# Performance work log

Hardware: AMD Instinct MI355X
Metric: run time of the kernel (lower is better)

## Reference

```python
import jax, jax.numpy as jnp
import numpy as np


def setup_inputs() -> dict:
    key = jax.random.key(0)
    kq, kk, kv, kl = jax.random.split(key, 4)
    B, H, S, D = 2, 8, 1024, 64
    Q = jax.random.normal(kq, (B, H, S, D), dtype=jnp.float32)
    K = jax.random.normal(kk, (B, H, S, D), dtype=jnp.float32)
    V = jax.random.normal(kv, (B, H, S, D), dtype=jnp.float32)
    valid_lens = jax.random.randint(kl, (B, S), 0, S, dtype=jnp.int64)
    return {"Q": Q, "K": K, "V": V, "valid_lens": valid_lens}


def reference(Q, K, V, valid_lens):
    # Q,K,V: [B,H,S,D]. The torch repeat/reshape makes K[b,i,j]=K[b,j],
    # i.e. every query head i attends to every key/value head j.
    B, H, S, D = Q.shape
    inv_sqrt = 1.0 / jnp.sqrt(jnp.asarray(D, dtype=Q.dtype))
    # score[b,i,j,s,t] = Q[b,i,s,:] . K[b,j,t,:] / sqrt(D)
    score = jnp.einsum('bisd,bjtd->bijst', Q, K) * inv_sqrt
    attention_weights = jax.nn.softmax(score, axis=-1)  # [B,H,H,S,S]
    # ctx[b,i,s,d] = sum_j sum_t w[b,i,j,s,t] * V[b,j,t,d]  (matmul then sum over j)
    ctx = jnp.einsum('bijst,bjtd->bisd', attention_weights, V)  # [B,H,S,D]
    context = jnp.transpose(ctx, (0, 2, 1, 3)).reshape(B, S, H * D)  # [B,S,H*D]
    return context, attention_weights
```

## Files before the change

kernel.cpp:

```cpp
#include <hip/hip_runtime.h>
#include <hip/hip_bf16.h>

#define B_ 2
#define H_ 8
#define S_ 1024
#define D_ 64
#define PLP 136
#define STRIPH (16 * PLP)

typedef short short8 __attribute__((ext_vector_type(8)));
typedef float f32x4 __attribute__((ext_vector_type(4)));

__device__ __forceinline__ unsigned int f2bf(float f) {
  union { float f; unsigned int u; } v; v.f = f;
  return (v.u + 0x7fffu + ((v.u >> 16) & 1u)) >> 16;
}
__device__ __forceinline__ float bf2f(unsigned int bits) {
  union { unsigned int u; float f; } v; v.u = bits << 16;
  return v.f;
}
__device__ __forceinline__ unsigned int cvt_pk_bf16(float lo, float hi) {
  unsigned int r;
  asm("v_cvt_pk_bf16_f32 %0, %1, %2" : "=v"(r) : "v"(lo), "v"(hi));
  return r;
}

__global__ void prologue_kernel(const float* __restrict__ Q,
                                const float* __restrict__ K,
                                const float* __restrict__ V,
                                unsigned short* __restrict__ Qb,
                                unsigned short* __restrict__ Kb,
                                unsigned short* __restrict__ Vt) {
  __shared__ float tile[64][65];
  const int bid = blockIdx.x;
  if (bid < 2048) {
    const float* src = (bid < 1024) ? Q : K;
    unsigned short* dst = (bid < 1024) ? Qb : Kb;
    int idx = (bid & 1023) * 256 + threadIdx.x;
    const float4 v = ((const float4*)src)[idx];
    unsigned int lo = f2bf(v.x) | (f2bf(v.y) << 16);
    unsigned int hi = f2bf(v.z) | (f2bf(v.w) << 16);
    ((uint2*)dst)[idx] = make_uint2(lo, hi);
    return;
  }
  const int tb = bid - 2048;
  int bh = tb >> 4;
  int t0 = (tb & 15) * 64;
  int tid = threadIdx.x;
  int cx = tid & 63, ry = tid >> 6;
  const float* src = V + ((size_t)bh * S_ + t0) * D_;
#pragma unroll
  for (int r = 0; r < 16; ++r) {
    int row = r * 4 + ry;
    tile[row][cx] = src[(size_t)row * D_ + cx];
  }
  __syncthreads();
  unsigned short* dst = Vt + (size_t)bh * D_ * S_ + t0;
#pragma unroll
  for (int r = 0; r < 16; ++r) {
    int d = r * 4 + ry;
    dst[(size_t)d * S_ + cx] = (unsigned short)f2bf(tile[cx][d]);
  }
}

__global__ __launch_bounds__(512, 2) void attn_kernel(
    const unsigned short* __restrict__ Qb,
    const unsigned short* __restrict__ Kb,
    const unsigned short* __restrict__ Vt,
    float* __restrict__ w_out,
    float* __restrict__ ctx_out)
{
  const int tid  = threadIdx.x;
  const int w    = tid >> 6;
  const int lane = tid & 63;
  const int g = lane >> 4;
  const int c = lane & 15;
  const int raw = blockIdx.x;
  const int bid = (raw & 7) * 32 + (raw >> 3);
  const int sb = bid & 15;
  const int i  = (bid >> 4) & 7;
  const int b  = bid >> 7;
  const int s0 = sb * 64;
  const int t0 = w * 128;

  __shared__ __align__(16) unsigned short pstrips[32 * STRIPH];
  __shared__ float ssum[2][8][64];
  unsigned short* stripA = pstrips + (4 * w) * STRIPH;
  unsigned short* stripB = stripA + STRIPH;
  unsigned short* stripC = stripB + STRIPH;
  unsigned short* stripD = stripC + STRIPH;

  const int l5  = lane >> 5;
  const int l31 = lane & 31;
  const int soff = l5 * PLP + l31 * 4;

  const unsigned short* qrow =
      Qb + ((size_t)((b * H_ + i) * S_) + s0 + c) * D_ + g * 8;
  short8 qa0 = *(const short8*)(qrow);
  short8 qa1 = *(const short8*)(qrow + 32);
  short8 qb0 = *(const short8*)(qrow + 16 * D_);
  short8 qb1 = *(const short8*)(qrow + 16 * D_ + 32);
  short8 qc0 = *(const short8*)(qrow + 32 * D_);
  short8 qc1 = *(const short8*)(qrow + 32 * D_ + 32);
  short8 qd0 = *(const short8*)(qrow + 48 * D_);
  short8 qd1 = *(const short8*)(qrow + 48 * D_ + 32);

  f32x4 ctxA[4], ctxB[4], ctxC[4], ctxD[4];
#pragma unroll
  for (int nt = 0; nt < 4; ++nt) {
    ctxA[nt] = (f32x4){0.f, 0.f, 0.f, 0.f};
    ctxB[nt] = (f32x4){0.f, 0.f, 0.f, 0.f};
    ctxC[nt] = (f32x4){0.f, 0.f, 0.f, 0.f};
    ctxD[nt] = (f32x4){0.f, 0.f, 0.f, 0.f};
  }

  const float SC = 0.18033688011112042f;

  for (int j = 0; j < H_; ++j) {
    const int par = j & 1;
    const unsigned short* kbase = Kb + (size_t)((b * H_ + j) * S_) * D_;

    float rsA = 0.f, rsB = 0.f, rsC = 0.f, rsD = 0.f;
#pragma unroll
    for (int tt = 0; tt < 8; ++tt) {
      const unsigned short* kr = kbase + (size_t)(t0 + tt * 16 + c) * D_ + g * 8;
      short8 kf0 = *(const short8*)(kr);
      short8 kf1 = *(const short8*)(kr + 32);
#define PASS1_HALF(QF0, QF1, RS, STRIPP)                                      \
      {                                                                       \
        f32x4 acc = (f32x4){0.f, 0.f, 0.f, 0.f};                              \
        acc = __builtin_amdgcn_mfma_f32_16x16x32_bf16(kf0, QF0, acc, 0, 0, 0);\
        acc = __builtin_amdgcn_mfma_f32_16x16x32_bf16(kf1, QF1, acc, 0, 0, 0);\
        float e0 = exp2f(acc[0] * SC);                                        \
        float e1 = exp2f(acc[1] * SC);                                        \
        float e2 = exp2f(acc[2] * SC);                                        \
        float e3 = exp2f(acc[3] * SC);                                        \
        RS += (e0 + e1) + (e2 + e3);                                          \
        uint2 pk = make_uint2(cvt_pk_bf16(e0, e1), cvt_pk_bf16(e2, e3));      \
        *(uint2*)&STRIPP[c * PLP + tt * 16 + 4 * g] = pk;                     \
      }
      PASS1_HALF(qa0, qa1, rsA, stripA)
      PASS1_HALF(qb0, qb1, rsB, stripB)
      PASS1_HALF(qc0, qc1, rsC, stripC)
      PASS1_HALF(qd0, qd1, rsD, stripD)
#undef PASS1_HALF
    }
    rsA += __shfl_xor(rsA, 16, 64);
    rsA += __shfl_xor(rsA, 32, 64);
    rsB += __shfl_xor(rsB, 16, 64);
    rsB += __shfl_xor(rsB, 32, 64);
    rsC += __shfl_xor(rsC, 16, 64);
    rsC += __shfl_xor(rsC, 32, 64);
    rsD += __shfl_xor(rsD, 16, 64);
    rsD += __shfl_xor(rsD, 32, 64);
    if (lane < 16) {
      ssum[par][w][lane]      = rsA;
      ssum[par][w][16 + lane] = rsB;
      ssum[par][w][32 + lane] = rsC;
      ssum[par][w][48 + lane] = rsD;
    }

    asm volatile("s_waitcnt lgkmcnt(0)\n\ts_barrier" ::: "memory");

#define ROWSUM(OFS)                                                           \
    (ssum[par][0][(OFS) + c] + ssum[par][1][(OFS) + c] +                      \
     ssum[par][2][(OFS) + c] + ssum[par][3][(OFS) + c] +                      \
     ssum[par][4][(OFS) + c] + ssum[par][5][(OFS) + c] +                      \
     ssum[par][6][(OFS) + c] + ssum[par][7][(OFS) + c])
    float iqA = 1.f / ROWSUM(0);
    float iqB = 1.f / ROWSUM(16);
    float iqC = 1.f / ROWSUM(32);
    float iqD = 1.f / ROWSUM(48);
#undef ROWSUM

    f32x4 pvA[4], pvB[4], pvC[4], pvD[4];
#pragma unroll
    for (int nt = 0; nt < 4; ++nt) {
      pvA[nt] = (f32x4){0.f, 0.f, 0.f, 0.f};
      pvB[nt] = (f32x4){0.f, 0.f, 0.f, 0.f};
      pvC[nt] = (f32x4){0.f, 0.f, 0.f, 0.f};
      pvD[nt] = (f32x4){0.f, 0.f, 0.f, 0.f};
    }
    const unsigned short* vbase =
        Vt + ((size_t)((b * H_ + j) * D_) + c) * S_ + t0 + g * 8;
    float* wlane = w_out +
        ((size_t)((b * H_ + i) * H_ + j) * S_ + s0) * S_ + t0 +
        (size_t)l5 * S_ + l31 * 4;
#pragma unroll
    for (int ch = 0; ch < 4; ++ch) {
      short8 paA = *(const short8*)&stripA[c * PLP + ch * 32 + g * 8];
      short8 paB = *(const short8*)&stripB[c * PLP + ch * 32 + g * 8];
      short8 paC = *(const short8*)&stripC[c * PLP + ch * 32 + g * 8];
      short8 paD = *(const short8*)&stripD[c * PLP + ch * 32 + g * 8];
#pragma unroll
      for (int nt = 0; nt < 4; ++nt) {
        short8 vf = *(const short8*)(vbase + (size_t)nt * 16 * S_ + ch * 32);
        pvA[nt] = __builtin_amdgcn_mfma_f32_16x16x32_bf16(paA, vf, pvA[nt], 0, 0, 0);
        pvB[nt] = __builtin_amdgcn_mfma_f32_16x16x32_bf16(paB, vf, pvB[nt], 0, 0, 0);
        pvC[nt] = __builtin_amdgcn_mfma_f32_16x16x32_bf16(paC, vf, pvC[nt], 0, 0, 0);
        pvD[nt] = __builtin_amdgcn_mfma_f32_16x16x32_bf16(paD, vf, pvD[nt], 0, 0, 0);
      }
      const float iqh = (ch == 0) ? iqA : (ch == 1) ? iqB : (ch == 2) ? iqC : iqD;
      const unsigned short* sh =
          (ch == 0) ? stripA : (ch == 1) ? stripB : (ch == 2) ? stripC : stripD;
      float* wch = wlane + (size_t)(ch * 16) * S_;
#pragma unroll
      for (int q = 0; q < 8; ++q) {
        float s0v = __uint_as_float(
            __builtin_amdgcn_readlane(__float_as_uint(iqh), 2 * q));
        float s1v = __uint_as_float(
            __builtin_amdgcn_readlane(__float_as_uint(iqh), 2 * q + 1));
        float iql = (lane & 32) ? s1v : s0v;
        uint2 pk = *(const uint2*)&sh[2 * q * PLP + soff];
        f32x4 ww;
        ww[0] = bf2f(pk.x & 0xffffu) * iql;
        ww[1] = bf2f(pk.x >> 16)     * iql;
        ww[2] = bf2f(pk.y & 0xffffu) * iql;
        ww[3] = bf2f(pk.y >> 16)     * iql;
        __builtin_nontemporal_store(ww, (f32x4*)(wch + (size_t)(2 * q) * S_));
      }
    }

#define CTX_SCALE(IQ, PV, CTX)                                                \
    {                                                                         \
      float r0 = __shfl(IQ, 4 * g + 0, 64);                                   \
      float r1 = __shfl(IQ, 4 * g + 1, 64);                                   \
      float r2 = __shfl(IQ, 4 * g + 2, 64);                                   \
      float r3 = __shfl(IQ, 4 * g + 3, 64);                                   \
      _Pragma("unroll")                                                       \
      for (int nt = 0; nt < 4; ++nt) {                                        \
        CTX[nt][0] += PV[nt][0] * r0;                                         \
        CTX[nt][1] += PV[nt][1] * r1;                                         \
        CTX[nt][2] += PV[nt][2] * r2;                                         \
        CTX[nt][3] += PV[nt][3] * r3;                                         \
      }                                                                       \
    }
    CTX_SCALE(iqA, pvA, ctxA)
    CTX_SCALE(iqB, pvB, ctxB)
    CTX_SCALE(iqC, pvC, ctxC)
    CTX_SCALE(iqD, pvD, ctxD)
#undef CTX_SCALE
  }

  __syncthreads();
  float (*ctile)[64][68] = (float(*)[64][68])pstrips;
#pragma unroll
  for (int nt = 0; nt < 4; ++nt)
#pragma unroll
    for (int r = 0; r < 4; ++r) {
      ctile[w][4 * g + r][nt * 16 + c]      = ctxA[nt][r];
      ctile[w][16 + 4 * g + r][nt * 16 + c] = ctxB[nt][r];
      ctile[w][32 + 4 * g + r][nt * 16 + c] = ctxC[nt][r];
      ctile[w][48 + 4 * g + r][nt * 16 + c] = ctxD[nt][r];
    }
  __syncthreads();
#pragma unroll
  for (int it = 0; it < 2; ++it) {
    const int slot = it * 512 + tid;
    const int r  = slot >> 4;
    const int d0 = (slot & 15) * 4;
    f32x4 s = *(const f32x4*)&ctile[0][r][d0];
#pragma unroll
    for (int e = 1; e < 8; ++e) s += *(const f32x4*)&ctile[e][r][d0];
    *(f32x4*)(ctx_out + ((size_t)(b * S_ + s0 + r) * (H_ * D_) + i * D_ + d0)) = s;
  }
}

extern "C" void kernel_launch(void* const* d_in, const int* in_sizes, int n_in,
                              void* d_out, int out_size, void* d_ws, size_t ws_size,
                              hipStream_t stream) {
  const float* Q = (const float*)d_in[0];
  const float* K = (const float*)d_in[1];
  const float* V = (const float*)d_in[2];

  const size_t nelem = (size_t)B_ * H_ * S_ * D_;
  float* outc = (float*)d_out;
  float* outw = outc + (size_t)B_ * S_ * H_ * D_;

  unsigned short* Qb = (unsigned short*)d_ws;
  unsigned short* Kb = Qb + nelem;
  unsigned short* Vt = Kb + nelem;

  prologue_kernel<<<2304, 256, 0, stream>>>(Q, K, V, Qb, Kb, Vt);
  attn_kernel<<<B_ * H_ * (S_ / 64), 512, 0, stream>>>(Qb, Kb, Vt, outw, outc);
}
```

Before: 141.2 us.

## Software-pipeline QK/exp of one row-half with PV and weight stores of other

Splits the 64 query rows of each block into two 32-row halves and restructures the head loop into two alternating slots. In each slot, the QK^T plus exp pass for one half (for the current or next key head) is interleaved with the PV MFMAs and the normalized attention-weight stores for the other half. A prologue computes the first half for head 0, and the row-sum buffers are double-buffered by parity. The aim is to overlap exp/MFMA work with the large global weight-store stream. The cost is twice as many barriers and one redundant QK pass for head 0 in the final slot.

```diff
diff --git a/kernel.cpp b/kernel.cpp
--- a/kernel.cpp
+++ b/kernel.cpp
@@ -84,7 +84,7 @@
   const int t0 = w * 128;
 
   __shared__ __align__(16) unsigned short pstrips[32 * STRIPH];
-  __shared__ float ssum[2][8][64];
+  __shared__ float ssum[2][8][32];
   unsigned short* stripA = pstrips + (4 * w) * STRIPH;
   unsigned short* stripB = stripA + STRIPH;
   unsigned short* stripC = stripB + STRIPH;
@@ -116,110 +116,56 @@
 
   const float SC = 0.18033688011112042f;
 
-  for (int j = 0; j < H_; ++j) {
-    const int par = j & 1;
-    const unsigned short* kbase = Kb + (size_t)((b * H_ + j) * S_) * D_;
-
-    float rsA = 0.f, rsB = 0.f, rsC = 0.f, rsD = 0.f;
-#pragma unroll
-    for (int tt = 0; tt < 8; ++tt) {
-      const unsigned short* kr = kbase + (size_t)(t0 + tt * 16 + c) * D_ + g * 8;
-      short8 kf0 = *(const short8*)(kr);
-      short8 kf1 = *(const short8*)(kr + 32);
-#define PASS1_HALF(QF0, QF1, RS, STRIPP)                                      \
-      {                                                                       \
-        f32x4 acc = (f32x4){0.f, 0.f, 0.f, 0.f};                              \
-        acc = __builtin_amdgcn_mfma_f32_16x16x32_bf16(kf0, QF0, acc, 0, 0, 0);\
-        acc = __builtin_amdgcn_mfma_f32_16x16x32_bf16(kf1, QF1, acc, 0, 0, 0);\
-        float e0 = exp2f(acc[0] * SC);                                        \
-        float e1 = exp2f(acc[1] * SC);                                        \
-        float e2 = exp2f(acc[2] * SC);                                        \
-        float e3 = exp2f(acc[3] * SC);                                        \
-        RS += (e0 + e1) + (e2 + e3);                                          \
-        uint2 pk = make_uint2(cvt_pk_bf16(e0, e1), cvt_pk_bf16(e2, e3));      \
-        *(uint2*)&STRIPP[c * PLP + tt * 16 + 4 * g] = pk;                     \
-      }
-      PASS1_HALF(qa0, qa1, rsA, stripA)
-      PASS1_HALF(qb0, qb1, rsB, stripB)
-      PASS1_HALF(qc0, qc1, rsC, stripC)
-      PASS1_HALF(qd0, qd1, rsD, stripD)
-#undef PASS1_HALF
-    }
-    rsA += __shfl_xor(rsA, 16, 64);
-    rsA += __shfl_xor(rsA, 32, 64);
-    rsB += __shfl_xor(rsB, 16, 64);
-    rsB += __shfl_xor(rsB, 32, 64);
-    rsC += __shfl_xor(rsC, 16, 64);
-    rsC += __shfl_xor(rsC, 32, 64);
-    rsD += __shfl_xor(rsD, 16, 64);
-    rsD += __shfl_xor(rsD, 32, 64);
-    if (lane < 16) {
-      ssum[par][w][lane]      = rsA;
-      ssum[par][w][16 + lane] = rsB;
-      ssum[par][w][32 + lane] = rsC;
-      ssum[par][w][48 + lane] = rsD;
-    }
-
-    asm volatile("s_waitcnt lgkmcnt(0)\n\ts_barrier" ::: "memory");
-
-#define ROWSUM(OFS)                                                           \
-    (ssum[par][0][(OFS) + c] + ssum[par][1][(OFS) + c] +                      \
-     ssum[par][2][(OFS) + c] + ssum[par][3][(OFS) + c] +                      \
-     ssum[par][4][(OFS) + c] + ssum[par][5][(OFS) + c] +                      \
-     ssum[par][6][(OFS) + c] + ssum[par][7][(OFS) + c])
-    float iqA = 1.f / ROWSUM(0);
-    float iqB = 1.f / ROWSUM(16);
-    float iqC = 1.f / ROWSUM(32);
-    float iqD = 1.f / ROWSUM(48);
-#undef ROWSUM
-
-    f32x4 pvA[4], pvB[4], pvC[4], pvD[4];
-#pragma unroll
-    for (int nt = 0; nt < 4; ++nt) {
-      pvA[nt] = (f32x4){0.f, 0.f, 0.f, 0.f};
-      pvB[nt] = (f32x4){0.f, 0.f, 0.f, 0.f};
-      pvC[nt] = (f32x4){0.f, 0.f, 0.f, 0.f};
-      pvD[nt] = (f32x4){0.f, 0.f, 0.f, 0.f};
-    }
-    const unsigned short* vbase =
-        Vt + ((size_t)((b * H_ + j) * D_) + c) * S_ + t0 + g * 8;
-    float* wlane = w_out +
-        ((size_t)((b * H_ + i) * H_ + j) * S_ + s0) * S_ + t0 +
-        (size_t)l5 * S_ + l31 * 4;
-#pragma unroll
-    for (int ch = 0; ch < 4; ++ch) {
-      short8 paA = *(const short8*)&stripA[c * PLP + ch * 32 + g * 8];
-      short8 paB = *(const short8*)&stripB[c * PLP + ch * 32 + g * 8];
-      short8 paC = *(const short8*)&stripC[c * PLP + ch * 32 + g * 8];
-      short8 paD = *(const short8*)&stripD[c * PLP + ch * 32 + g * 8];
-#pragma unroll
-      for (int nt = 0; nt < 4; ++nt) {
-        short8 vf = *(const short8*)(vbase + (size_t)nt * 16 * S_ + ch * 32);
-        pvA[nt] = __builtin_amdgcn_mfma_f32_16x16x32_bf16(paA, vf, pvA[nt], 0, 0, 0);
-        pvB[nt] = __builtin_amdgcn_mfma_f32_16x16x32_bf16(paB, vf, pvB[nt], 0, 0, 0);
-        pvC[nt] = __builtin_amdgcn_mfma_f32_16x16x32_bf16(paC, vf, pvC[nt], 0, 0, 0);
-        pvD[nt] = __builtin_amdgcn_mfma_f32_16x16x32_bf16(paD, vf, pvD[nt], 0, 0, 0);
-      }
-      const float iqh = (ch == 0) ? iqA : (ch == 1) ? iqB : (ch == 2) ? iqC : iqD;
-      const unsigned short* sh =
-          (ch == 0) ? stripA : (ch == 1) ? stripB : (ch == 2) ? stripC : stripD;
-      float* wch = wlane + (size_t)(ch * 16) * S_;
-#pragma unroll
-      for (int q = 0; q < 8; ++q) {
-        float s0v = __uint_as_float(
-            __builtin_amdgcn_readlane(__float_as_uint(iqh), 2 * q));
-        float s1v = __uint_as_float(
-            __builtin_amdgcn_readlane(__float_as_uint(iqh), 2 * q + 1));
-        float iql = (lane & 32) ? s1v : s0v;
-        uint2 pk = *(const uint2*)&sh[2 * q * PLP + soff];
-        f32x4 ww;
-        ww[0] = bf2f(pk.x & 0xffffu) * iql;
-        ww[1] = bf2f(pk.x >> 16)     * iql;
-        ww[2] = bf2f(pk.y & 0xffffu) * iql;
-        ww[3] = bf2f(pk.y >> 16)     * iql;
-        __builtin_nontemporal_store(ww, (f32x4*)(wch + (size_t)(2 * q) * S_));
-      }
-    }
+#define PASS1_SUB(KF0, KF1, QF0, QF1, RS, STRIPP, TT)                         \
+  {                                                                           \
+    f32x4 acc = (f32x4){0.f, 0.f, 0.f, 0.f};                                  \
+    acc = __builtin_amdgcn_mfma_f32_16x16x32_bf16(KF0, QF0, acc, 0, 0, 0);    \
+    acc = __builtin_amdgcn_mfma_f32_16x16x32_bf16(KF1, QF1, acc, 0, 0, 0);    \
+    float e0 = exp2f(acc[0] * SC);                                            \
+    float e1 = exp2f(acc[1] * SC);                                            \
+    float e2 = exp2f(acc[2] * SC);                                            \
+    float e3 = exp2f(acc[3] * SC);                                            \
+    RS += (e0 + e1) + (e2 + e3);                                              \
+    uint2 pk = make_uint2(cvt_pk_bf16(e0, e1), cvt_pk_bf16(e2, e3));          \
+    *(uint2*)&STRIPP[c * PLP + (TT) * 16 + 4 * g] = pk;                       \
+  }
+
+#define PVS_CHUNK(CH, SV0, SV1, PV0, PV1, IQ0, IQ1, VB, WL)                   \
+  {                                                                           \
+    short8 pa0 = *(const short8*)&SV0[c * PLP + (CH) * 32 + g * 8];           \
+    short8 pa1 = *(const short8*)&SV1[c * PLP + (CH) * 32 + g * 8];           \
+    _Pragma("unroll")                                                         \
+    for (int nt = 0; nt < 4; ++nt) {                                          \
+      short8 vf = *(const short8*)((VB) + (size_t)nt * 16 * S_ + (CH) * 32);  \
+      PV0[nt] = __builtin_amdgcn_mfma_f32_16x16x32_bf16(pa0, vf, PV0[nt], 0, 0, 0); \
+      PV1[nt] = __builtin_amdgcn_mfma_f32_16x16x32_bf16(pa1, vf, PV1[nt], 0, 0, 0); \
+    }                                                                         \
+    const unsigned short* sh_ = ((CH) < 2) ? (SV0) : (SV1);                   \
+    const float iqh_ = ((CH) < 2) ? (IQ0) : (IQ1);                            \
+    _Pragma("unroll")                                                         \
+    for (int q = 0; q < 4; ++q) {                                             \
+      const int rr = ((CH) & 1) * 8 + 2 * q;                                  \
+      float s0v = __uint_as_float(                                            \
+          __builtin_amdgcn_readlane(__float_as_uint(iqh_), rr));              \
+      float s1v = __uint_as_float(                                            \
+          __builtin_amdgcn_readlane(__float_as_uint(iqh_), rr + 1));          \
+      float iql = (lane & 32) ? s1v : s0v;                                    \
+      uint2 pk = *(const uint2*)&sh_[rr * PLP + soff];                        \
+      f32x4 ww;                                                               \
+      ww[0] = bf2f(pk.x & 0xffffu) * iql;                                     \
+      ww[1] = bf2f(pk.x >> 16)     * iql;                                     \
+      ww[2] = bf2f(pk.y & 0xffffu) * iql;                                     \
+      ww[3] = bf2f(pk.y >> 16)     * iql;                                     \
+      __builtin_nontemporal_store(ww,                                         \
+          (f32x4*)((WL) + (size_t)(((CH) < 2 ? 0 : 16) + rr) * S_));          \
+    }                                                                         \
+  }
+
+#define ROWSUM(PAR, OFS)                                                      \
+    (ssum[PAR][0][(OFS) + c] + ssum[PAR][1][(OFS) + c] +                      \
+     ssum[PAR][2][(OFS) + c] + ssum[PAR][3][(OFS) + c] +                      \
+     ssum[PAR][4][(OFS) + c] + ssum[PAR][5][(OFS) + c] +                      \
+     ssum[PAR][6][(OFS) + c] + ssum[PAR][7][(OFS) + c])
 
 #define CTX_SCALE(IQ, PV, CTX)                                                \
     {                                                                         \
@@ -235,12 +181,84 @@
         CTX[nt][3] += PV[nt][3] * r3;                                         \
       }                                                                       \
     }
-    CTX_SCALE(iqA, pvA, ctxA)
-    CTX_SCALE(iqB, pvB, ctxB)
-    CTX_SCALE(iqC, pvC, ctxC)
-    CTX_SCALE(iqD, pvD, ctxD)
+
+#define SLOT(JP, QP00, QP01, QP10, QP11, SP0, SP1, PARP,                      \
+             JV, SV0, SV1, CTX0, CTX1, PARV, ROWB)                            \
+  {                                                                           \
+    float fs0 = ROWSUM(PARV, 0), fs1 = ROWSUM(PARV, 16);                      \
+    float iq0 = 1.f / fs0, iq1 = 1.f / fs1;                                   \
+    f32x4 pv0[4], pv1[4];                                                     \
+    _Pragma("unroll")                                                         \
+    for (int nt = 0; nt < 4; ++nt) {                                          \
+      pv0[nt] = (f32x4){0.f, 0.f, 0.f, 0.f};                                  \
+      pv1[nt] = (f32x4){0.f, 0.f, 0.f, 0.f};                                  \
+    }                                                                         \
+    const unsigned short* kbase = Kb + (size_t)((b * H_ + (JP)) * S_) * D_;   \
+    const unsigned short* vbase =                                             \
+        Vt + ((size_t)((b * H_ + (JV)) * D_) + c) * S_ + t0 + g * 8;          \
+    float* wlane = w_out +                                                    \
+        ((size_t)((b * H_ + i) * H_ + (JV)) * S_ + s0 + (ROWB)) * S_ + t0 +   \
+        (size_t)l5 * S_ + l31 * 4;                                            \
+    float rs0 = 0.f, rs1 = 0.f;                                               \
+    _Pragma("unroll")                                                         \
+    for (int tt = 0; tt < 8; ++tt) {                                          \
+      const unsigned short* kr =                                              \
+          kbase + (size_t)(t0 + tt * 16 + c) * D_ + g * 8;                    \
+      short8 kf0 = *(const short8*)(kr);                                      \
+      short8 kf1 = *(const short8*)(kr + 32);                                 \
+      PASS1_SUB(kf0, kf1, QP00, QP01, rs0, SP0, tt)                           \
+      PASS1_SUB(kf0, kf1, QP10, QP11, rs1, SP1, tt)                           \
+      if (tt & 1) {                                                           \
+        PVS_CHUNK(tt >> 1, SV0, SV1, pv0, pv1, iq0, iq1, vbase, wlane)        \
+      }                                                                       \
+    }                                                                         \
+    rs0 += __shfl_xor(rs0, 16, 64);                                           \
+    rs0 += __shfl_xor(rs0, 32, 64);                                           \
+    rs1 += __shfl_xor(rs1, 16, 64);                                           \
+    rs1 += __shfl_xor(rs1, 32, 64);                                           \
+    if (lane < 16) {                                                          \
+      ssum[PARP][w][lane] = rs0;                                              \
+      ssum[PARP][w][16 + lane] = rs1;                                         \
+    }                                                                         \
+    CTX_SCALE(iq0, pv0, CTX0)                                                 \
+    CTX_SCALE(iq1, pv1, CTX1)                                                 \
+    asm volatile("s_waitcnt lgkmcnt(0)\n\ts_barrier" ::: "memory");           \
+  }
+
+  {
+    const unsigned short* kbase = Kb + (size_t)((b * H_ + 0) * S_) * D_;
+    float rs0 = 0.f, rs1 = 0.f;
+#pragma unroll
+    for (int tt = 0; tt < 8; ++tt) {
+      const unsigned short* kr =
+          kbase + (size_t)(t0 + tt * 16 + c) * D_ + g * 8;
+      short8 kf0 = *(const short8*)(kr);
+      short8 kf1 = *(const short8*)(kr + 32);
+      PASS1_SUB(kf0, kf1, qa0, qa1, rs0, stripA, tt)
+      PASS1_SUB(kf0, kf1, qb0, qb1, rs1, stripB, tt)
+    }
+    rs0 += __shfl_xor(rs0, 16, 64);
+    rs0 += __shfl_xor(rs0, 32, 64);
+    rs1 += __shfl_xor(rs1, 16, 64);
+    rs1 += __shfl_xor(rs1, 32, 64);
+    if (lane < 16) {
+      ssum[0][w][lane] = rs0;
+      ssum[0][w][16 + lane] = rs1;
+    }
+    asm volatile("s_waitcnt lgkmcnt(0)\n\ts_barrier" ::: "memory");
+  }
+
+  for (int j = 0; j < H_; ++j) {
+    SLOT(j, qc0, qc1, qd0, qd1, stripC, stripD, 1,
+         j, stripA, stripB, ctxA, ctxB, 0, 0)
+    SLOT((j + 1) & 7, qa0, qa1, qb0, qb1, stripA, stripB, 0,
+         j, stripC, stripD, ctxC, ctxD, 1, 32)
+  }
+#undef SLOT
 #undef CTX_SCALE
-  }
+#undef ROWSUM
+#undef PVS_CHUNK
+#undef PASS1_SUB
 
   __syncthreads();
   float (*ctile)[64][68] = (float(*)[64][68])pstrips;
```

Result: slower. 166.3 us (+17.8%).
